# Optimization experiments

Hardware: AMD Instinct MI355X
Metric: run time of the kernel (lower is better)

## Reference

```python
import jax, jax.numpy as jnp
import numpy as np
from jax.scipy.special import logsumexp

EXPERT_NUM = 64
MOE_TOPK = 2

def setup_inputs() -> dict:
    key = jax.random.key(0)
    k1, k2 = jax.random.split(key)
    x = jax.random.normal(k1, (4, 4096, 4096), dtype=jnp.float32)
    # nn.Linear(input_size, expert_num).weight has shape [expert_num, input_size]
    W = jax.random.normal(k2, (EXPERT_NUM, 4096), dtype=jnp.float32) * (1.0 / np.sqrt(4096))
    return {"x": x, "W": W}

def reference(x, W):
    # logits: [B, S, E]
    logits = jnp.einsum('bsd,ed->bse', x, W)
    k = min(MOE_TOPK + 1, EXPERT_NUM)  # torch takes topk+1 then slices
    topk_logits, topk_indices = jax.lax.top_k(logits, k)
    topk_logits = topk_logits[..., :MOE_TOPK]     # [B, S, K]
    topk_indices = topk_indices[..., :MOE_TOPK]   # [B, S, K]
    # regularized=True: softmax over the top-k logits in float32
    topk_scores = jax.nn.softmax(topk_logits.astype(jnp.float32), axis=-1).astype(logits.dtype)
    # scatter into zeros; topk indices are unique so one-hot sum == scatter-set
    scores_filtered = jnp.sum(
        jax.nn.one_hot(topk_indices, EXPERT_NUM, dtype=logits.dtype) * topk_scores[..., None],
        axis=-2)  # [B, S, E]
    # router_z loss, per-token [B, S]
    log_z = logsumexp(logits, axis=-1)
    loss = log_z ** 2
    return logits, scores_filtered, loss
```

## Files before the change

### kernel.cpp

```cpp
#include <hip/hip_runtime.h>
#include <math.h>

#define TTOK 16384
#define DD   4096
#define EE   64
#define TM   32
#define BK   64
#define NCH  (DD / BK)

typedef __attribute__((ext_vector_type(8))) short short8;
typedef __attribute__((ext_vector_type(4))) float f32x4;

static __device__ __forceinline__ unsigned short f2bf(float f) {
    unsigned u = __float_as_uint(f);
    u += 0x7FFFu + ((u >> 16) & 1u);
    return (unsigned short)(u >> 16);
}
static __device__ __forceinline__ float bf2f(unsigned short h) {
    return __uint_as_float(((unsigned)h) << 16);
}
static __device__ __forceinline__ void cvt8(float4 a, float4 b, short8& hi, short8& lo) {
    const float v[8] = {a.x, a.y, a.z, a.w, b.x, b.y, b.z, b.w};
#pragma unroll
    for (int j = 0; j < 8; ++j) {
        const unsigned short h = f2bf(v[j]);
        hi[j] = (short)h;
        lo[j] = (short)f2bf(v[j] - bf2f(h));
    }
}

__global__ void w_convert(const float* __restrict__ W,
                          unsigned short* __restrict__ whi,
                          unsigned short* __restrict__ wlo) {
    const int i = (blockIdx.x * blockDim.x + threadIdx.x) * 4;
    if (i >= EE * DD) return;
    const float4 v = *reinterpret_cast<const float4*>(W + i);
    ushort4 h, l;
    h.x = f2bf(v.x); l.x = f2bf(v.x - bf2f(h.x));
    h.y = f2bf(v.y); l.y = f2bf(v.y - bf2f(h.y));
    h.z = f2bf(v.z); l.z = f2bf(v.z - bf2f(h.z));
    h.w = f2bf(v.w); l.w = f2bf(v.w - bf2f(h.w));
    *reinterpret_cast<ushort4*>(whi + i) = h;
    *reinterpret_cast<ushort4*>(wlo + i) = l;
}

__global__ __launch_bounds__(256, 2)
void moe_fused(const float* __restrict__ x,
               const unsigned short* __restrict__ whi,
               const unsigned short* __restrict__ wlo,
               float* __restrict__ out)
{
    __shared__ unsigned short xh[TM * 64];
    __shared__ unsigned short xl[TM * 64];
    __shared__ unsigned short whs[EE * 64];
    __shared__ unsigned short wls[EE * 64];
    __shared__ float lg[TM * 68];

    const int tid  = threadIdx.x;
    const int wv   = tid >> 6;
    const int lane = tid & 63;
    const int m    = lane & 15;
    const int q    = lane >> 4;
    const int tg   = wv >> 1;
    const int eh   = wv & 1;
    const int t0   = blockIdx.x * TM;

    const int sr = tid >> 3;
    const int sj = tid & 7;
    const int sp  = (sj ^ (sr & 7)) * 8;
    const int xo  = sr * 64 + sp;
    const int wo0 = xo;
    const int wo1 = (sr + 32) * 64 + sp;

    const float*          gx  = x   + (size_t)(t0 + sr) * DD + sj * 8;
    const unsigned short* gh0 = whi + (size_t)sr * DD + sj * 8;
    const unsigned short* gh1 = gh0 + (size_t)32 * DD;
    const unsigned short* gl0 = wlo + (size_t)sr * DD + sj * 8;
    const unsigned short* gl1 = gl0 + (size_t)32 * DD;

    f32x4 acc0 = (f32x4){0.f, 0.f, 0.f, 0.f};
    f32x4 acc1 = (f32x4){0.f, 0.f, 0.f, 0.f};

    float4 fx0  = *reinterpret_cast<const float4*>(gx);
    float4 fx1  = *reinterpret_cast<const float4*>(gx + 4);
    short8 pwh0 = *reinterpret_cast<const short8*>(gh0);
    short8 pwh1 = *reinterpret_cast<const short8*>(gh1);
    short8 pwl0 = *reinterpret_cast<const short8*>(gl0);
    short8 pwl1 = *reinterpret_cast<const short8*>(gl1);

    const int sa  = m & 7;
    const int ra  = (16 * tg + m) * 64;
    const int rb0 = (32 * eh + m) * 64;
    const int rb1 = (32 * eh + 16 + m) * 64;

    for (int kc = 0; kc < NCH; ++kc) {
        __syncthreads();
        {
            short8 h, l;
            cvt8(fx0, fx1, h, l);
            *reinterpret_cast<short8*>(xh + xo)   = h;
            *reinterpret_cast<short8*>(xl + xo)   = l;
            *reinterpret_cast<short8*>(whs + wo0) = pwh0;
            *reinterpret_cast<short8*>(whs + wo1) = pwh1;
            *reinterpret_cast<short8*>(wls + wo0) = pwl0;
            *reinterpret_cast<short8*>(wls + wo1) = pwl1;
        }
        __syncthreads();

        if (kc + 1 < NCH) {
            const int off = (kc + 1) * BK;
            fx0  = *reinterpret_cast<const float4*>(gx + off);
            fx1  = *reinterpret_cast<const float4*>(gx + off + 4);
            pwh0 = *reinterpret_cast<const short8*>(gh0 + off);
            pwh1 = *reinterpret_cast<const short8*>(gh1 + off);
            pwl0 = *reinterpret_cast<const short8*>(gl0 + off);
            pwl1 = *reinterpret_cast<const short8*>(gl1 + off);
        }

#pragma unroll
        for (int kss = 0; kss < 2; ++kss) {
            const int ca = ((4 * kss + q) ^ sa) * 8;
            const short8 ah  = *reinterpret_cast<const short8*>(xh + ra + ca);
            const short8 al  = *reinterpret_cast<const short8*>(xl + ra + ca);
            const short8 bh0 = *reinterpret_cast<const short8*>(whs + rb0 + ca);
            const short8 bl0 = *reinterpret_cast<const short8*>(wls + rb0 + ca);
            const short8 bh1 = *reinterpret_cast<const short8*>(whs + rb1 + ca);
            const short8 bl1 = *reinterpret_cast<const short8*>(wls + rb1 + ca);
            acc0 = __builtin_amdgcn_mfma_f32_16x16x32_bf16(ah, bh0, acc0, 0, 0, 0);
            acc0 = __builtin_amdgcn_mfma_f32_16x16x32_bf16(ah, bl0, acc0, 0, 0, 0);
            acc0 = __builtin_amdgcn_mfma_f32_16x16x32_bf16(al, bh0, acc0, 0, 0, 0);
            acc1 = __builtin_amdgcn_mfma_f32_16x16x32_bf16(ah, bh1, acc1, 0, 0, 0);
            acc1 = __builtin_amdgcn_mfma_f32_16x16x32_bf16(ah, bl1, acc1, 0, 0, 0);
            acc1 = __builtin_amdgcn_mfma_f32_16x16x32_bf16(al, bh1, acc1, 0, 0, 0);
        }
    }

    {
        float* lr = lg + (16 * tg + 4 * q) * 68 + 32 * eh + m;
#pragma unroll
        for (int i = 0; i < 4; ++i) {
            lr[i * 68]      = acc0[i];
            lr[i * 68 + 16] = acc1[i];
        }
    }
    __syncthreads();

    const int tt = tid >> 3;
    const int j  = tid & 3 ? (tid & 7) : (tid & 7);
    const float* row = lg + tt * 68 + (tid & 7) * 8;
    const int jj = tid & 7;
    const float4 lv0 = *reinterpret_cast<const float4*>(row);
    const float4 lv1 = *reinterpret_cast<const float4*>(row + 4);
    const float r[8] = {lv0.x, lv0.y, lv0.z, lv0.w, lv1.x, lv1.y, lv1.z, lv1.w};
    (void)j;

    float* gout = out + (size_t)(t0 + tt) * EE + jj * 8;
    *reinterpret_cast<float4*>(gout)     = lv0;
    *reinterpret_cast<float4*>(gout + 4) = lv1;

    float v1 = -INFINITY, v2 = -INFINITY;
    int   i1 = 0, i2 = 0;
#pragma unroll
    for (int c = 0; c < 8; ++c) {
        const int e = jj * 8 + c;
        const float v = r[c];
        if (v > v1)      { v2 = v1; i2 = i1; v1 = v; i1 = e; }
        else if (v > v2) { v2 = v;  i2 = e; }
    }
#pragma unroll
    for (int mk = 1; mk < 8; mk <<= 1) {
        const float ov1 = __shfl_xor(v1, mk);
        const int   oi1 = __shfl_xor(i1, mk);
        const float ov2 = __shfl_xor(v2, mk);
        const int   oi2 = __shfl_xor(i2, mk);
        const bool aw = (v1 > ov1) || (v1 == ov1 && i1 < oi1);
        const float c1v = aw ? v1 : ov1;  const int c1i = aw ? i1 : oi1;
        const float cav = aw ? v2 : ov2;  const int cai = aw ? i2 : oi2;
        const float cbv = aw ? ov1 : v1;  const int cbi = aw ? oi1 : i1;
        const bool bw = (cav > cbv) || (cav == cbv && cai < cbi);
        v1 = c1v; i1 = c1i;
        v2 = bw ? cav : cbv;
        i2 = bw ? cai : cbi;
    }

    float sm = 0.f;
#pragma unroll
    for (int c = 0; c < 8; ++c) sm += expf(r[c] - v1);
#pragma unroll
    for (int mk = 1; mk < 8; mk <<= 1) sm += __shfl_xor(sm, mk);

    const float logz = v1 + logf(sm);
    if (jj == 0) out[(size_t)2 * TTOK * EE + t0 + tt] = logz * logz;

    const float e21 = expf(v2 - v1);
    const float rr  = 1.f / (1.f + e21);
    const float s1 = rr, s2 = e21 * rr;
    float* sc = out + (size_t)TTOK * EE + (size_t)(t0 + tt) * EE + jj * 8;
    float vv[8];
#pragma unroll
    for (int c = 0; c < 8; ++c) {
        const int e = jj * 8 + c;
        vv[c] = (e == i1) ? s1 : ((e == i2) ? s2 : 0.f);
    }
    *reinterpret_cast<float4*>(sc)     = make_float4(vv[0], vv[1], vv[2], vv[3]);
    *reinterpret_cast<float4*>(sc + 4) = make_float4(vv[4], vv[5], vv[6], vv[7]);
}

extern "C" void kernel_launch(void* const* d_in, const int* in_sizes, int n_in,
                              void* d_out, int out_size, void* d_ws, size_t ws_size,
                              hipStream_t stream) {
    const float* x = (const float*)d_in[0];
    const float* W = (const float*)d_in[1];
    float* out = (float*)d_out;
    unsigned short* whi = (unsigned short*)d_ws;
    unsigned short* wlo = whi + (size_t)EE * DD;

    w_convert<<<dim3((EE * DD / 4 + 255) / 256), dim3(256), 0, stream>>>(W, whi, wlo);
    moe_fused<<<dim3(TTOK / TM), dim3(256), 0, stream>>>(x, whi, wlo, out);
}
```

Before: 383.3 us.

## Stream pre-swizzled weight chunks directly into double-buffered LDS via async global loads

The weight conversion kernel now writes the hi/lo bf16 weights in a chunk-major, pre-swizzled layout that matches the LDS tile. The main kernel fetches each next weight chunk with global_load_lds directly into a second LDS buffer, so those loads no longer pass through registers or need explicit LDS stores. This is meant to cut VGPR pressure and ds_write traffic and to overlap weight fetch with MFMA work. It doubles weight LDS usage and relies on the compiler's vmcnt waits for the x loads to also cover the async LDS loads.

```diff
diff --git a/kernel.cpp b/kernel.cpp
--- a/kernel.cpp
+++ b/kernel.cpp
@@ -7,6 +7,7 @@
 #define TM   32
 #define BK   64
 #define NCH  (DD / BK)
+#define WCH  (EE * BK)
 
 typedef __attribute__((ext_vector_type(8))) short short8;
 typedef __attribute__((ext_vector_type(4))) float f32x4;
@@ -29,19 +30,28 @@
     }
 }
 
+static __device__ __forceinline__ void gload16(const unsigned short* g, unsigned short* l) {
+    __builtin_amdgcn_global_load_lds(
+        (const __attribute__((address_space(1))) unsigned int*)g,
+        (__attribute__((address_space(3))) unsigned int*)l, 16, 0, 0);
+}
+
 __global__ void w_convert(const float* __restrict__ W,
                           unsigned short* __restrict__ whi,
                           unsigned short* __restrict__ wlo) {
-    const int i = (blockIdx.x * blockDim.x + threadIdx.x) * 4;
-    if (i >= EE * DD) return;
-    const float4 v = *reinterpret_cast<const float4*>(W + i);
-    ushort4 h, l;
-    h.x = f2bf(v.x); l.x = f2bf(v.x - bf2f(h.x));
-    h.y = f2bf(v.y); l.y = f2bf(v.y - bf2f(h.y));
-    h.z = f2bf(v.z); l.z = f2bf(v.z - bf2f(h.z));
-    h.w = f2bf(v.w); l.w = f2bf(v.w - bf2f(h.w));
-    *reinterpret_cast<ushort4*>(whi + i) = h;
-    *reinterpret_cast<ushort4*>(wlo + i) = l;
+    const int t  = blockIdx.x * blockDim.x + threadIdx.x;
+    const int r  = t >> 9;
+    const int g  = t & 511;
+    const int kc = g >> 3;
+    const int j  = g & 7;
+    const float* src = W + (size_t)r * DD + kc * BK + j * 8;
+    const float4 a = *reinterpret_cast<const float4*>(src);
+    const float4 b = *reinterpret_cast<const float4*>(src + 4);
+    short8 h, l;
+    cvt8(a, b, h, l);
+    const int slot = kc * 512 + r * 8 + (j ^ (r & 7));
+    *reinterpret_cast<short8*>(whi + (size_t)slot * 8) = h;
+    *reinterpret_cast<short8*>(wlo + (size_t)slot * 8) = l;
 }
 
 __global__ __launch_bounds__(256, 2)
@@ -52,8 +62,8 @@
 {
     __shared__ unsigned short xh[TM * 64];
     __shared__ unsigned short xl[TM * 64];
-    __shared__ unsigned short whs[EE * 64];
-    __shared__ unsigned short wls[EE * 64];
+    __shared__ unsigned short whs[2 * WCH];
+    __shared__ unsigned short wls[2 * WCH];
     __shared__ float lg[TM * 68];
 
     const int tid  = threadIdx.x;
@@ -67,26 +77,22 @@
 
     const int sr = tid >> 3;
     const int sj = tid & 7;
-    const int sp  = (sj ^ (sr & 7)) * 8;
-    const int xo  = sr * 64 + sp;
-    const int wo0 = xo;
-    const int wo1 = (sr + 32) * 64 + sp;
-
-    const float*          gx  = x   + (size_t)(t0 + sr) * DD + sj * 8;
-    const unsigned short* gh0 = whi + (size_t)sr * DD + sj * 8;
-    const unsigned short* gh1 = gh0 + (size_t)32 * DD;
-    const unsigned short* gl0 = wlo + (size_t)sr * DD + sj * 8;
-    const unsigned short* gl1 = gl0 + (size_t)32 * DD;
+    const int xo = sr * 64 + (sj ^ (sr & 7)) * 8;
+    const float* gx = x + (size_t)(t0 + sr) * DD + sj * 8;
+
+    const int ws0 = wv * 64 + lane;
+    const int ws1 = 256 + ws0;
 
     f32x4 acc0 = (f32x4){0.f, 0.f, 0.f, 0.f};
     f32x4 acc1 = (f32x4){0.f, 0.f, 0.f, 0.f};
 
-    float4 fx0  = *reinterpret_cast<const float4*>(gx);
-    float4 fx1  = *reinterpret_cast<const float4*>(gx + 4);
-    short8 pwh0 = *reinterpret_cast<const short8*>(gh0);
-    short8 pwh1 = *reinterpret_cast<const short8*>(gh1);
-    short8 pwl0 = *reinterpret_cast<const short8*>(gl0);
-    short8 pwl1 = *reinterpret_cast<const short8*>(gl1);
+    gload16(whi + (size_t)ws0 * 8, whs + ws0 * 8);
+    gload16(whi + (size_t)ws1 * 8, whs + ws1 * 8);
+    gload16(wlo + (size_t)ws0 * 8, wls + ws0 * 8);
+    gload16(wlo + (size_t)ws1 * 8, wls + ws1 * 8);
+    __builtin_amdgcn_sched_barrier(0);
+    float4 fx0 = *reinterpret_cast<const float4*>(gx);
+    float4 fx1 = *reinterpret_cast<const float4*>(gx + 4);
 
     const int sa  = m & 7;
     const int ra  = (16 * tg + m) * 64;
@@ -94,38 +100,45 @@
     const int rb1 = (32 * eh + 16 + m) * 64;
 
     for (int kc = 0; kc < NCH; ++kc) {
-        __syncthreads();
+        __builtin_amdgcn_s_barrier();
+        __builtin_amdgcn_sched_barrier(0);
+        if (kc + 1 < NCH) {
+            const int nb = ((kc + 1) & 1) * WCH;
+            const unsigned short* gh = whi + (size_t)(kc + 1) * WCH;
+            const unsigned short* gl = wlo + (size_t)(kc + 1) * WCH;
+            gload16(gh + (size_t)ws0 * 8, whs + nb + ws0 * 8);
+            gload16(gh + (size_t)ws1 * 8, whs + nb + ws1 * 8);
+            gload16(gl + (size_t)ws0 * 8, wls + nb + ws0 * 8);
+            gload16(gl + (size_t)ws1 * 8, wls + nb + ws1 * 8);
+        }
+        __builtin_amdgcn_sched_barrier(0);
+
         {
             short8 h, l;
             cvt8(fx0, fx1, h, l);
-            *reinterpret_cast<short8*>(xh + xo)   = h;
-            *reinterpret_cast<short8*>(xl + xo)   = l;
-            *reinterpret_cast<short8*>(whs + wo0) = pwh0;
-            *reinterpret_cast<short8*>(whs + wo1) = pwh1;
-            *reinterpret_cast<short8*>(wls + wo0) = pwl0;
-            *reinterpret_cast<short8*>(wls + wo1) = pwl1;
-        }
-        __syncthreads();
-
+            *reinterpret_cast<short8*>(xh + xo) = h;
+            *reinterpret_cast<short8*>(xl + xo) = l;
+        }
         if (kc + 1 < NCH) {
             const int off = (kc + 1) * BK;
-            fx0  = *reinterpret_cast<const float4*>(gx + off);
-            fx1  = *reinterpret_cast<const float4*>(gx + off + 4);
-            pwh0 = *reinterpret_cast<const short8*>(gh0 + off);
-            pwh1 = *reinterpret_cast<const short8*>(gh1 + off);
-            pwl0 = *reinterpret_cast<const short8*>(gl0 + off);
-            pwl1 = *reinterpret_cast<const short8*>(gl1 + off);
-        }
-
+            fx0 = *reinterpret_cast<const float4*>(gx + off);
+            fx1 = *reinterpret_cast<const float4*>(gx + off + 4);
+        }
+
+        asm volatile("s_waitcnt lgkmcnt(0)" ::: "memory");
+        __builtin_amdgcn_s_barrier();
+        __builtin_amdgcn_sched_barrier(0);
+
+        const int cb = (kc & 1) * WCH;
 #pragma unroll
         for (int kss = 0; kss < 2; ++kss) {
             const int ca = ((4 * kss + q) ^ sa) * 8;
             const short8 ah  = *reinterpret_cast<const short8*>(xh + ra + ca);
             const short8 al  = *reinterpret_cast<const short8*>(xl + ra + ca);
-            const short8 bh0 = *reinterpret_cast<const short8*>(whs + rb0 + ca);
-            const short8 bl0 = *reinterpret_cast<const short8*>(wls + rb0 + ca);
-            const short8 bh1 = *reinterpret_cast<const short8*>(whs + rb1 + ca);
-            const short8 bl1 = *reinterpret_cast<const short8*>(wls + rb1 + ca);
+            const short8 bh0 = *reinterpret_cast<const short8*>(whs + cb + rb0 + ca);
+            const short8 bl0 = *reinterpret_cast<const short8*>(wls + cb + rb0 + ca);
+            const short8 bh1 = *reinterpret_cast<const short8*>(whs + cb + rb1 + ca);
+            const short8 bl1 = *reinterpret_cast<const short8*>(wls + cb + rb1 + ca);
             acc0 = __builtin_amdgcn_mfma_f32_16x16x32_bf16(ah, bh0, acc0, 0, 0, 0);
             acc0 = __builtin_amdgcn_mfma_f32_16x16x32_bf16(ah, bl0, acc0, 0, 0, 0);
             acc0 = __builtin_amdgcn_mfma_f32_16x16x32_bf16(al, bh0, acc0, 0, 0, 0);
@@ -146,13 +159,11 @@
     __syncthreads();
 
     const int tt = tid >> 3;
-    const int j  = tid & 3 ? (tid & 7) : (tid & 7);
-    const float* row = lg + tt * 68 + (tid & 7) * 8;
     const int jj = tid & 7;
+    const float* row = lg + tt * 68 + jj * 8;
     const float4 lv0 = *reinterpret_cast<const float4*>(row);
     const float4 lv1 = *reinterpret_cast<const float4*>(row + 4);
     const float r[8] = {lv0.x, lv0.y, lv0.z, lv0.w, lv1.x, lv1.y, lv1.z, lv1.w};
-    (void)j;
 
     float* gout = out + (size_t)(t0 + tt) * EE + jj * 8;
     *reinterpret_cast<float4*>(gout)     = lv0;
@@ -194,13 +205,13 @@
 
     const float e21 = expf(v2 - v1);
     const float rr  = 1.f / (1.f + e21);
-    const float s1 = rr, s2 = e21 * rr;
+    const float sc1 = rr, sc2 = e21 * rr;
     float* sc = out + (size_t)TTOK * EE + (size_t)(t0 + tt) * EE + jj * 8;
     float vv[8];
 #pragma unroll
     for (int c = 0; c < 8; ++c) {
         const int e = jj * 8 + c;
-        vv[c] = (e == i1) ? s1 : ((e == i2) ? s2 : 0.f);
+        vv[c] = (e == i1) ? sc1 : ((e == i2) ? sc2 : 0.f);
     }
     *reinterpret_cast<float4*>(sc)     = make_float4(vv[0], vv[1], vv[2], vv[3]);
     *reinterpret_cast<float4*>(sc + 4) = make_float4(vv[4], vv[5], vv[6], vv[7]);
@@ -215,6 +226,6 @@
     unsigned short* whi = (unsigned short*)d_ws;
     unsigned short* wlo = whi + (size_t)EE * DD;
 
-    w_convert<<<dim3((EE * DD / 4 + 255) / 256), dim3(256), 0, stream>>>(W, whi, wlo);
+    w_convert<<<dim3(EE * DD / 8 / 256), dim3(256), 0, stream>>>(W, whi, wlo);
     moe_fused<<<dim3(TTOK / TM), dim3(256), 0, stream>>>(x, whi, wlo, out);
 }
```

New measurement: 383.8 us. About the same (+0.1%).
